# Performance work log

Measured on AMD Instinct MI355X. Metric: run time of the kernel, lower is better.

## Reference

```python
import jax, jax.numpy as jnp
import numpy as np

N_NODES = 100000
N_EDGES = 600000
D = 128          # encoder_output_dim
H = 64           # mlp_edge_model_dim


def setup_inputs() -> dict:
    key = jax.random.key(0)
    k1, k2, k3, k4, k5, k6 = jax.random.split(key, 6)
    node_emb = jax.random.normal(k1, (N_NODES, D), dtype=jnp.float32)
    edge_index = jax.random.randint(k2, (2, N_EDGES), 0, N_NODES, dtype=jnp.int64)
    # MLP params (Linear(2D -> H), Linear(H -> 1)); scale ~ PyTorch default init
    s1 = 1.0 / np.sqrt(2 * D)
    s2 = 1.0 / np.sqrt(H)
    W1 = jax.random.uniform(k3, (2 * D, H), dtype=jnp.float32, minval=-s1, maxval=s1)
    b1 = jax.random.uniform(k4, (H,), dtype=jnp.float32, minval=-s1, maxval=s1)
    W2 = jax.random.uniform(k5, (H, 1), dtype=jnp.float32, minval=-s2, maxval=s2)
    b2 = jax.random.uniform(k6, (1,), dtype=jnp.float32, minval=-s2, maxval=s2)
    return {"node_emb": node_emb, "edge_index": edge_index,
            "W1": W1, "b1": b1, "W2": W2, "b2": b2}


def reference(node_emb, edge_index, W1, b1, W2, b2):
    src, dst = edge_index[0], edge_index[1]
    emb_src = node_emb[src]                      # [E, D] gather
    emb_dst = node_emb[dst]                      # [E, D] gather
    edge_emb = jnp.concatenate([emb_src, emb_dst], axis=1)  # [E, 2D]
    h = jax.nn.relu(edge_emb @ W1 + b1)          # [E, H]
    edge_logits = h @ W2 + b2                    # [E, 1]
    return edge_logits
```

## Files before the change

kernel.cpp:

```cpp
#include <hip/hip_runtime.h>
#include <hip/hip_fp16.h>

#define N_NODES 100000
#define N_EDGES 600000
#define DIM 128
#define HID 64
#define NCHUNK 1563

typedef __attribute__((ext_vector_type(8))) _Float16 half8;
typedef __attribute__((ext_vector_type(4))) _Float16 half4v;
typedef __attribute__((ext_vector_type(4))) float floatx4;

__device__ __forceinline__ void gload_lds16(const void* g, void* l) {
    __builtin_amdgcn_global_load_lds(
        (const __attribute__((address_space(1))) void*)g,
        (__attribute__((address_space(3))) void*)l, 16, 0, 0);
}

__global__ __launch_bounds__(256) void prep_W(
    const float* __restrict__ W1, __half* __restrict__ W1T)
{
    const int o = (int)(blockIdx.x * blockDim.x + threadIdx.x) * 2;
    if (o >= 128 * 128) return;
    const int c = o >> 7, k = o & 127;
    float w0, w1;
    if (c < HID) { w0 = W1[k * HID + c];               w1 = W1[(k + 1) * HID + c]; }
    else         { w0 = W1[(DIM + k) * HID + c - HID]; w1 = W1[(DIM + k + 1) * HID + c - HID]; }
    W1T[o]     = __float2half(w0);
    W1T[o + 1] = __float2half(w1);
}

__global__ __launch_bounds__(256, 2) void precompute_P(
    const float* __restrict__ node_emb,
    const __half* __restrict__ W1T,
    const float* __restrict__ b1,
    __half* __restrict__ P)
{
    __shared__ float Abuf[2][64 * 128];

    const int tid  = threadIdx.x;
    const int w    = tid >> 6;
    const int lane = tid & 63;
    const int lr   = lane & 15;
    const int q    = lane >> 4;

    half8 wf[8][4];
#pragma unroll
    for (int nt = 0; nt < 8; nt++)
#pragma unroll
        for (int ks = 0; ks < 4; ks++)
            wf[nt][ks] = *(const half8*)(W1T + (size_t)(nt * 16 + lr) * 128 + ks * 32 + q * 8);

    float bias_[4][4];
#pragma unroll
    for (int nt = 0; nt < 4; nt++) {
        const float4 b4 = *(const float4*)(b1 + nt * 16 + q * 4);
        bias_[nt][0] = b4.x; bias_[nt][1] = b4.y;
        bias_[nt][2] = b4.z; bias_[nt][3] = b4.w;
    }

    const int r8   = tid >> 5;
    const int in16 = (tid & 31) << 4;
    const char* nb = (const char*)node_emb;

    int c = (int)blockIdx.x;
#pragma unroll
    for (int r = 0; r < 8; r++) {
        int row_in = r * 8 + r8;
        int grow = c * 64 + row_in;
        if (grow >= N_NODES) grow = N_NODES - 1;
        const size_t src = (size_t)grow * 512 + (size_t)(in16 ^ ((row_in & 7) << 4));
        gload_lds16(nb + src, (char*)&Abuf[0][0] + (r * 4096 + tid * 16));
    }

    int cur = 0;
    for (; c < NCHUNK; c += (int)gridDim.x, cur ^= 1) {
        const int cnext = c + (int)gridDim.x;
        if (cnext < NCHUNK) {
#pragma unroll
            for (int r = 0; r < 8; r++) {
                int row_in = r * 8 + r8;
                int grow = cnext * 64 + row_in;
                if (grow >= N_NODES) grow = N_NODES - 1;
                const size_t src = (size_t)grow * 512 + (size_t)(in16 ^ ((row_in & 7) << 4));
                gload_lds16(nb + src, (char*)&Abuf[cur ^ 1][0] + (r * 4096 + tid * 16));
            }
            asm volatile("s_waitcnt vmcnt(8)" ::: "memory");
        } else {
            asm volatile("s_waitcnt vmcnt(0)" ::: "memory");
        }
        __builtin_amdgcn_s_barrier();

        floatx4 acc[8];
#pragma unroll
        for (int nt = 0; nt < 8; nt++) acc[nt] = (floatx4){0.f, 0.f, 0.f, 0.f};

        const char* Ab = (const char*)&Abuf[cur][0];
        const int rb = w * 16 + lr;
        const int sw = (rb & 7) << 4;
#pragma unroll
        for (int ks = 0; ks < 4; ks++) {
            const int cb = ks * 128 + q * 32;
            const float4 x0 = *(const float4*)(Ab + rb * 512 + ((cb)      ^ sw));
            const float4 x1 = *(const float4*)(Ab + rb * 512 + ((cb + 16) ^ sw));
            half8 af;
            af[0] = (_Float16)x0.x; af[1] = (_Float16)x0.y;
            af[2] = (_Float16)x0.z; af[3] = (_Float16)x0.w;
            af[4] = (_Float16)x1.x; af[5] = (_Float16)x1.y;
            af[6] = (_Float16)x1.z; af[7] = (_Float16)x1.w;
#pragma unroll
            for (int nt = 0; nt < 8; nt++)
                acc[nt] = __builtin_amdgcn_mfma_f32_16x16x32_f16(wf[nt][ks], af, acc[nt], 0, 0, 0);
        }

        const int grow = c * 64 + w * 16 + lr;
        if (grow < N_NODES) {
            char* prow = (char*)P + (size_t)grow * 256;
#pragma unroll
            for (int m = 0; m < 4; m++) {
                half8 hh;
#pragma unroll
                for (int i = 0; i < 4; i++) {
                    float va = acc[2 * m][i];
                    float vb = acc[2 * m + 1][i];
                    if (m < 2) {
                        va += bias_[2 * m][i];
                        vb += bias_[2 * m + 1][i];
                    }
                    hh[i]     = (_Float16)va;
                    hh[i + 4] = (_Float16)vb;
                }
                *(half8*)(prow + m * 64 + q * 16) = hh;
            }
        }
        __builtin_amdgcn_s_barrier();
    }
}

__device__ inline bool detect_int64(const int* e32) {
    int orv = 0;
#pragma unroll
    for (int k = 0; k < 8; k++) orv |= e32[2 * k + 1];
    return orv == 0;
}

__global__ __launch_bounds__(256) void edge_mlp(
    const __half* __restrict__ P,
    const void* __restrict__ eidx_raw,
    const float* __restrict__ W2,
    const float* __restrict__ b2,
    float* __restrict__ out)
{
    const int* e32 = (const int*)eidx_raw;
    const long long* e64 = (const long long*)eidx_raw;
    const bool is64 = detect_int64(e32);

    const int tid  = threadIdx.x;
    const int lane = tid & 63;
    const int j    = lane & 15;
    const int grp  = lane >> 4;
    const int hbase = ((j >> 3) << 5) + ((j & 1) << 4) + (((j >> 1) & 3) << 2);
    const float4 w2 = *(const float4*)(W2 + hbase);
    const float b2v = b2[0];

    const int gwid   = (int)((blockIdx.x * blockDim.x + tid) >> 6);
    const int nwaves = (int)((gridDim.x * blockDim.x) >> 6);

    const half4v zero = {(_Float16)0, (_Float16)0, (_Float16)0, (_Float16)0};

    for (int base = gwid * 16; base < N_EDGES; base += nwaves * 16) {
        int s[4], d[4];
#pragma unroll
        for (int u = 0; u < 4; u++) {
            const int e = base + 4 * u + grp;
            if (is64) { s[u] = (int)e64[e]; d[u] = (int)e64[N_EDGES + e]; }
            else      { s[u] = e32[e];      d[u] = e32[N_EDGES + e]; }
        }
        half4v av[4], bv[4];
#pragma unroll
        for (int u = 0; u < 4; u++) {
            av[u] = *(const half4v*)(P + (size_t)s[u] * 128 + 4 * j);
            bv[u] = *(const half4v*)(P + (size_t)d[u] * 128 + 64 + 4 * j);
        }
#pragma unroll
        for (int u = 0; u < 4; u++) {
            const half4v t = av[u] + bv[u];
            const half4v r = __builtin_elementwise_max(t, zero);
            float acc = (float)r[0] * w2.x + (float)r[1] * w2.y
                      + (float)r[2] * w2.z + (float)r[3] * w2.w;
#pragma unroll
            for (int off = 8; off >= 1; off >>= 1)
                acc += __shfl_xor(acc, off, 64);
            if (j == 0) out[base + 4 * u + grp] = acc + b2v;
        }
    }
}

__global__ __launch_bounds__(256) void edge_mlp_direct(
    const float* __restrict__ node_emb,
    const void* __restrict__ eidx_raw,
    const float* __restrict__ W1,
    const float* __restrict__ b1,
    const float* __restrict__ W2,
    const float* __restrict__ b2,
    float* __restrict__ out)
{
    const int* e32 = (const int*)eidx_raw;
    const long long* e64 = (const long long*)eidx_raw;
    const bool is64 = detect_int64(e32);

    const int lane = threadIdx.x & 63;
    const float w2  = W2[lane];
    const float b2v = b2[0];
    const int gwid   = (int)((blockIdx.x * blockDim.x + threadIdx.x) >> 6);
    const int nwaves = (int)((gridDim.x * blockDim.x) >> 6);

    for (int e = gwid; e < N_EDGES; e += nwaves) {
        int s, d;
        if (is64) { s = (int)e64[e]; d = (int)e64[N_EDGES + e]; }
        else      { s = e32[e];      d = e32[N_EDGES + e]; }
        const float* es = node_emb + (size_t)s * DIM;
        const float* ed = node_emb + (size_t)d * DIM;
        float acc = b1[lane];
        for (int k = 0; k < DIM; k++) {
            acc += es[k] * W1[k * HID + lane];
            acc += ed[k] * W1[(DIM + k) * HID + lane];
        }
        float t = fmaxf(acc, 0.f) * w2;
#pragma unroll
        for (int off = 32; off >= 1; off >>= 1)
            t += __shfl_xor(t, off, 64);
        if (lane == 0) out[e] = t + b2v;
    }
}

extern "C" void kernel_launch(void* const* d_in, const int* in_sizes, int n_in,
                              void* d_out, int out_size, void* d_ws, size_t ws_size,
                              hipStream_t stream) {
    const float* node_emb = (const float*)d_in[0];
    const void*  eidx     = d_in[1];
    const float* W1       = (const float*)d_in[2];
    const float* b1       = (const float*)d_in[3];
    const float* W2       = (const float*)d_in[4];
    const float* b2       = (const float*)d_in[5];
    float* out = (float*)d_out;

    const size_t wt_off = 32u * 1024 * 1024;
    const size_t need   = wt_off + 128 * 128 * sizeof(__half);

    if (ws_size >= need) {
        __half* P   = (__half*)d_ws;
        __half* W1T = (__half*)((char*)d_ws + wt_off);
        prep_W<<<32, 256, 0, stream>>>(W1, W1T);
        precompute_P<<<512, 256, 0, stream>>>(node_emb, W1T, b1, P);
        edge_mlp<<<2048, 256, 0, stream>>>(P, eidx, W2, b2, out);
    } else {
        edge_mlp_direct<<<4096, 256, 0, stream>>>(node_emb, eidx, W1, b1, W2, b2, out);
    }
}
```

Before: 51.18 us.

## Give each wave its own double-buffered tile pipeline and drop block barriers in precompute_P

Result: no change. 51.57 us (+0.8%).

```diff
diff --git a/kernel.cpp b/kernel.cpp
--- a/kernel.cpp
+++ b/kernel.cpp
@@ -5,11 +5,13 @@
 #define N_EDGES 600000
 #define DIM 128
 #define HID 64
-#define NCHUNK 1563
+#define NTILES 6250
 
 typedef __attribute__((ext_vector_type(8))) _Float16 half8;
 typedef __attribute__((ext_vector_type(4))) _Float16 half4v;
 typedef __attribute__((ext_vector_type(4))) float floatx4;
+
+#define VMCNT(n) asm volatile("s_waitcnt vmcnt(" #n ")" ::: "memory")
 
 __device__ __forceinline__ void gload_lds16(const void* g, void* l) {
     __builtin_amdgcn_global_load_lds(
@@ -36,7 +38,7 @@
     const float* __restrict__ b1,
     __half* __restrict__ P)
 {
-    __shared__ float Abuf[2][64 * 128];
+    __shared__ char lds[4][2][8192];
 
     const int tid  = threadIdx.x;
     const int w    = tid >> 6;
@@ -59,50 +61,52 @@
         bias_[nt][2] = b4.z; bias_[nt][3] = b4.w;
     }
 
-    const int r8   = tid >> 5;
-    const int in16 = (tid & 31) << 4;
+    const int b     = (int)blockIdx.x;
+    const int base  = b * 12 + (b < 106 ? b : 106);
+    const int quota = 12 + (b < 106 ? 1 : 0);
+
     const char* nb = (const char*)node_emb;
-
-    int c = (int)blockIdx.x;
-#pragma unroll
-    for (int r = 0; r < 8; r++) {
-        int row_in = r * 8 + r8;
-        int grow = c * 64 + row_in;
-        if (grow >= N_NODES) grow = N_NODES - 1;
-        const size_t src = (size_t)grow * 512 + (size_t)(in16 ^ ((row_in & 7) << 4));
-        gload_lds16(nb + src, (char*)&Abuf[0][0] + (r * 4096 + tid * 16));
-    }
+    char* const bufs[2] = { &lds[w][0][0], &lds[w][1][0] };
+
+    const int rhalf = lane >> 5;
+    const int in16  = (lane & 31) << 4;
+
+#define STAGE(T, BUF)                                                        \
+    {                                                                        \
+        _Pragma("unroll")                                                    \
+        for (int r = 0; r < 8; r++) {                                        \
+            const int row_in = 2 * r + rhalf;                                \
+            const size_t src = (size_t)((T) * 16 + row_in) * 512             \
+                             + (size_t)(in16 ^ ((row_in & 7) << 4));         \
+            gload_lds16(nb + src, (BUF) + r * 1024);                         \
+        }                                                                    \
+    }
+
+    int i  = w;
+    int tA = (i     < quota) ? base + i     : -1;
+    int tB = (i + 4 < quota) ? base + i + 4 : -1;
+    int nexti = i + 8;
+
+    if (tA >= 0) STAGE(tA, bufs[0]);
+    if (tB >= 0) STAGE(tB, bufs[1]);
 
     int cur = 0;
-    for (; c < NCHUNK; c += (int)gridDim.x, cur ^= 1) {
-        const int cnext = c + (int)gridDim.x;
-        if (cnext < NCHUNK) {
-#pragma unroll
-            for (int r = 0; r < 8; r++) {
-                int row_in = r * 8 + r8;
-                int grow = cnext * 64 + row_in;
-                if (grow >= N_NODES) grow = N_NODES - 1;
-                const size_t src = (size_t)grow * 512 + (size_t)(in16 ^ ((row_in & 7) << 4));
-                gload_lds16(nb + src, (char*)&Abuf[cur ^ 1][0] + (r * 4096 + tid * 16));
-            }
-            asm volatile("s_waitcnt vmcnt(8)" ::: "memory");
-        } else {
-            asm volatile("s_waitcnt vmcnt(0)" ::: "memory");
-        }
-        __builtin_amdgcn_s_barrier();
+    bool first = true;
+    while (tA >= 0) {
+        if (first) { if (tB >= 0) VMCNT(8);  else VMCNT(0); }
+        else       { if (tB >= 0) VMCNT(12); else VMCNT(4); }
 
         floatx4 acc[8];
 #pragma unroll
         for (int nt = 0; nt < 8; nt++) acc[nt] = (floatx4){0.f, 0.f, 0.f, 0.f};
 
-        const char* Ab = (const char*)&Abuf[cur][0];
-        const int rb = w * 16 + lr;
-        const int sw = (rb & 7) << 4;
+        const char* Ab = bufs[cur];
+        const int sw = (lr & 7) << 4;
 #pragma unroll
         for (int ks = 0; ks < 4; ks++) {
             const int cb = ks * 128 + q * 32;
-            const float4 x0 = *(const float4*)(Ab + rb * 512 + ((cb)      ^ sw));
-            const float4 x1 = *(const float4*)(Ab + rb * 512 + ((cb + 16) ^ sw));
+            const float4 x0 = *(const float4*)(Ab + lr * 512 + ((cb)      ^ sw));
+            const float4 x1 = *(const float4*)(Ab + lr * 512 + ((cb + 16) ^ sw));
             half8 af;
             af[0] = (_Float16)x0.x; af[1] = (_Float16)x0.y;
             af[2] = (_Float16)x0.z; af[3] = (_Float16)x0.w;
@@ -113,28 +117,32 @@
                 acc[nt] = __builtin_amdgcn_mfma_f32_16x16x32_f16(wf[nt][ks], af, acc[nt], 0, 0, 0);
         }
 
-        const int grow = c * 64 + w * 16 + lr;
-        if (grow < N_NODES) {
-            char* prow = (char*)P + (size_t)grow * 256;
+        asm volatile("s_waitcnt lgkmcnt(0)" ::: "memory");
+        __builtin_amdgcn_sched_barrier(0);
+
+        const int tC = (nexti < quota) ? base + nexti : -1;
+        if (tC >= 0) STAGE(tC, bufs[cur]);
+
+        {
+            char* prow = (char*)P + (size_t)(tA * 16 + lr) * 256;
 #pragma unroll
             for (int m = 0; m < 4; m++) {
                 half8 hh;
 #pragma unroll
-                for (int i = 0; i < 4; i++) {
-                    float va = acc[2 * m][i];
-                    float vb = acc[2 * m + 1][i];
-                    if (m < 2) {
-                        va += bias_[2 * m][i];
-                        vb += bias_[2 * m + 1][i];
-                    }
-                    hh[i]     = (_Float16)va;
-                    hh[i + 4] = (_Float16)vb;
+                for (int ii = 0; ii < 4; ii++) {
+                    float va = acc[2 * m][ii];
+                    float vb = acc[2 * m + 1][ii];
+                    if (m < 2) { va += bias_[2 * m][ii]; vb += bias_[2 * m + 1][ii]; }
+                    hh[ii]     = (_Float16)va;
+                    hh[ii + 4] = (_Float16)vb;
                 }
                 *(half8*)(prow + m * 64 + q * 16) = hh;
             }
         }
-        __builtin_amdgcn_s_barrier();
-    }
+
+        tA = tB; tB = tC; nexti += 4; cur ^= 1; first = false;
+    }
+#undef STAGE
 }
 
 __device__ inline bool detect_int64(const int* e32) {
```
